# Kernel tuning notes

Hardware: AMD Instinct MI355X
Metric: run time of the kernel (lower is better)

Reference implementation:

```python
import jax, jax.numpy as jnp
import numpy as np

NUM_EMBEDDINGS = 1024
EMBEDDING_DIM = 256
COMMITMENT_COST = 0.25


def setup_inputs() -> dict:
    key = jax.random.key(0)
    k1, k2 = jax.random.split(key)
    inputs = jax.random.normal(k1, (32, EMBEDDING_DIM, 32, 32), dtype=jnp.float32)
    # codebook init matches torch: uniform(-1/K, 1/K)
    weight = jax.random.uniform(
        k2, (NUM_EMBEDDINGS, EMBEDDING_DIM), dtype=jnp.float32,
        minval=-1.0 / NUM_EMBEDDINGS, maxval=1.0 / NUM_EMBEDDINGS)
    return {"inputs": inputs, "weight": weight}


def reference(inputs, weight):
    # inputs: [B, C, H, W] with C == EMBEDDING_DIM; weight: [K, D]
    x = jnp.transpose(inputs, (0, 2, 3, 1))            # [B, H, W, D]
    input_shape = x.shape
    flat = x.reshape(-1, EMBEDDING_DIM)                # [N, D]

    distances = (jnp.sum(flat * flat, axis=1, keepdims=True)
                 + jnp.sum(weight * weight, axis=1)
                 - 2.0 * (flat @ weight.T))
    encoding_indices = jnp.argmin(distances, axis=1)   # [N]
    encodings = jax.nn.one_hot(encoding_indices, NUM_EMBEDDINGS, dtype=jnp.float32)  # [N, K]

    # one_hot @ weight == gather; use gather for efficiency (same values)
    quantized = weight[encoding_indices].reshape(input_shape)  # [B, H, W, D]

    e_latent_loss = jnp.mean((jax.lax.stop_gradient(quantized) - x) ** 2)
    q_latent_loss = jnp.mean((quantized - jax.lax.stop_gradient(x)) ** 2)
    loss = q_latent_loss + COMMITMENT_COST * e_latent_loss

    # straight-through estimator
    quantized_st = x + jax.lax.stop_gradient(quantized - x)

    avg_probs = jnp.mean(encodings, axis=0)            # [K]
    perplexity = jnp.exp(-jnp.sum(avg_probs * jnp.log(avg_probs + 1e-10)))

    return (loss,
            jnp.transpose(quantized_st, (0, 3, 1, 2)),  # back to [B, C, H, W]
            perplexity,
            encodings)
```

## Files before the change

kernel.cpp:

```cpp
#include <hip/hip_runtime.h>
#include <hip/hip_bf16.h>

#define HWDIM 1024
#define DDIM 256
#define KCODES 1024
#define NROWS 32768
#define BSTRIDE (DDIM * HWDIM)
#define GUARD 1.5e-4f

typedef __attribute__((ext_vector_type(8))) short short8;
typedef __attribute__((ext_vector_type(4))) float f32x4;
typedef unsigned long long ull;


__device__ __forceinline__ unsigned short f2bf(float v) {
  __hip_bfloat16 b = __float2bfloat16(v);
  return *reinterpret_cast<unsigned short*>(&b);
}
__device__ __forceinline__ float bf2f(unsigned short u) {
  __hip_bfloat16 b;
  *reinterpret_cast<unsigned short*>(&b) = u;
  return __bfloat162float(b);
}
__device__ __forceinline__ ull pk(float d, int k) {
  unsigned ub = __float_as_uint(d);
  ub = (ub & 0x80000000u) ? ~ub : (ub | 0x80000000u);
  return ((ull)ub << 32) | (unsigned)k;
}
__device__ __forceinline__ float keyq(ull key) {
  unsigned ub = (unsigned)(key >> 32);
  unsigned orig = (ub & 0x80000000u) ? (ub & 0x7FFFFFFFu) : ~ub;
  return __uint_as_float(orig);
}

__device__ __forceinline__ float pair128_sq(const float* p, int stride) {
  float a[8];
#pragma unroll
  for (int j = 0; j < 8; ++j) { float v = p[j * stride]; a[j] = __fmul_rn(v, v); }
  for (int i = 8; i < 128; i += 8) {
#pragma unroll
    for (int j = 0; j < 8; ++j) {
      float v = p[(i + j) * stride];
      a[j] = __fadd_rn(a[j], __fmul_rn(v, v));
    }
  }
  float s01 = __fadd_rn(a[0], a[1]), s23 = __fadd_rn(a[2], a[3]);
  float s45 = __fadd_rn(a[4], a[5]), s67 = __fadd_rn(a[6], a[7]);
  return __fadd_rn(__fadd_rn(s01, s23), __fadd_rn(s45, s67));
}

__global__ __launch_bounds__(256) void k_prep(
    const float* __restrict__ w, float* __restrict__ wT, float* __restrict__ ss,
    int* __restrict__ hist, double* __restrict__ loss,
    int* __restrict__ wcount, int* __restrict__ pcount,
    unsigned short* __restrict__ wh8, unsigned short* __restrict__ wl8) {
  __shared__ float tile[64][65];
  const int t = threadIdx.x;
  int g = blockIdx.x * 256 + t;
  {
    int k = g >> 5, oct = g & 31;
    const float* p = w + k * DDIM + oct * 8;
    short8 hv, lv;
#pragma unroll
    for (int j = 0; j < 8; ++j) {
      float v = p[j];
      unsigned short h = f2bf(v);
      unsigned short l = f2bf(__fsub_rn(v, bf2f(h)));
      hv[j] = (short)h; lv[j] = (short)l;
    }
    *(short8*)&wh8[oct * 8192 + k * 8] = hv;
    *(short8*)&wl8[oct * 8192 + k * 8] = lv;
  }
  if (g < KCODES) {
    hist[g] = 0;
    const float* p = w + g * DDIM;
    ss[g] = __fadd_rn(pair128_sq(p, 1), pair128_sq(p + 128, 1));
  }
  if (g == 0) { *loss = 0.0; *wcount = 0; *pcount = 0; }
  if (blockIdx.x < 64) {
    const int k0 = (blockIdx.x & 15) * 64, d0 = (blockIdx.x >> 4) * 64;
    const int c = t & 63, r = t >> 6;
#pragma unroll
    for (int m = 0; m < 16; ++m)
      tile[r + m * 4][c] = w[(k0 + r + m * 4) * DDIM + d0 + c];
    __syncthreads();
#pragma unroll
    for (int m = 0; m < 16; ++m)
      wT[(size_t)(d0 + r + m * 4) * KCODES + k0 + c] = tile[c][r + m * 4];
  }
}

__global__ __launch_bounds__(256) void k_argmfma(
    const float* __restrict__ in,
    const unsigned short* __restrict__ wh8, const unsigned short* __restrict__ wl8,
    const float* __restrict__ ss, unsigned* __restrict__ kkarr,
    int* __restrict__ wlist, int* __restrict__ wcount,
    int* __restrict__ plist, int* __restrict__ pcount) {
  __shared__ __align__(16) unsigned short Ah[32 * 64 * 8];
  __shared__ __align__(16) unsigned short Al[32 * 64 * 8];
  __shared__ ull best1[64], best2[64], best3[64];

  const int t = threadIdx.x;
  const int n0 = blockIdx.x * 64;
  const int b = n0 >> 10, hw0 = n0 & 1023;

  {
    const int hw = t & 63, dg = t >> 6;
    const float* xp = in + b * BSTRIDE + hw0 + hw;
#pragma unroll
    for (int dd = 0; dd < 64; dd += 2) {
      int d = dg * 64 + dd;
      float f0 = xp[d * HWDIM], f1 = xp[(d + 1) * HWDIM];
      unsigned short h0 = f2bf(f0);
      unsigned short l0 = f2bf(__fsub_rn(f0, bf2f(h0)));
      unsigned short h1 = f2bf(f1);
      unsigned short l1 = f2bf(__fsub_rn(f1, bf2f(h1)));
      int base = ((d >> 3) * 64 + hw) * 8 + (d & 7);
      *(unsigned*)&Ah[base] = (unsigned)h0 | ((unsigned)h1 << 16);
      *(unsigned*)&Al[base] = (unsigned)l0 | ((unsigned)l1 << 16);
    }
  }
  if (t < 64) { best1[t] = ~0ull; best2[t] = ~0ull; best3[t] = ~0ull; }
  __syncthreads();

  const int wv = t >> 6, ln = t & 63;
  const int rw = (wv & 1) * 32;
  const int cw = (wv >> 1) * 64;
  const int l15 = ln & 15, quad = ln >> 4;

  ull rb1[8], rb2[8], rb3[8];
#pragma unroll
  for (int i = 0; i < 8; ++i) { rb1[i] = ~0ull; rb2[i] = ~0ull; rb3[i] = ~0ull; }

  for (int kb = 0; kb < 8; ++kb) {
    const int cb = kb * 128 + cw;
    f32x4 acc[2][4];
#pragma unroll
    for (int rt = 0; rt < 2; ++rt)
#pragma unroll
      for (int ct = 0; ct < 4; ++ct) acc[rt][ct] = (f32x4){0.f, 0.f, 0.f, 0.f};

#pragma unroll
    for (int ki = 0; ki < 8; ++ki) {
      const int obase = ki * 4 + quad;
      short8 ah[2], al[2], bh[4], bl[4];
#pragma unroll
      for (int rt = 0; rt < 2; ++rt) {
        int row = rw + rt * 16 + l15;
        ah[rt] = *(const short8*)&Ah[(obase * 64 + row) * 8];
        al[rt] = *(const short8*)&Al[(obase * 64 + row) * 8];
      }
#pragma unroll
      for (int ct = 0; ct < 4; ++ct) {
        int off = obase * 8192 + (cb + ct * 16 + l15) * 8;
        bh[ct] = *(const short8*)&wh8[off];
        bl[ct] = *(const short8*)&wl8[off];
      }
#pragma unroll
      for (int rt = 0; rt < 2; ++rt)
#pragma unroll
        for (int ct = 0; ct < 4; ++ct) {
          acc[rt][ct] = __builtin_amdgcn_mfma_f32_16x16x32_bf16(ah[rt], bh[ct], acc[rt][ct], 0, 0, 0);
          acc[rt][ct] = __builtin_amdgcn_mfma_f32_16x16x32_bf16(ah[rt], bl[ct], acc[rt][ct], 0, 0, 0);
          acc[rt][ct] = __builtin_amdgcn_mfma_f32_16x16x32_bf16(al[rt], bh[ct], acc[rt][ct], 0, 0, 0);
        }
    }

    float sv[4];
#pragma unroll
    for (int ct = 0; ct < 4; ++ct) sv[ct] = ss[cb + ct * 16 + l15];
#pragma unroll
    for (int rt = 0; rt < 2; ++rt)
#pragma unroll
      for (int reg = 0; reg < 4; ++reg) {
        int idx = rt * 4 + reg;
        ull b1 = rb1[idx], b2 = rb2[idx], b3 = rb3[idx];
#pragma unroll
        for (int ct = 0; ct < 4; ++ct) {
          float q = fmaf(-2.f, acc[rt][ct][reg], sv[ct]);
          ull key = pk(q, cb + ct * 16 + l15);
          if (key < b1)      { b3 = b2; b2 = b1; b1 = key; }
          else if (key < b2) { b3 = b2; b2 = key; }
          else if (key < b3) { b3 = key; }
        }
        rb1[idx] = b1; rb2[idx] = b2; rb3[idx] = b3;
      }
  }

#pragma unroll
  for (int rt = 0; rt < 2; ++rt)
#pragma unroll
    for (int reg = 0; reg < 4; ++reg)
      atomicMin(&best1[rw + rt * 16 + quad * 4 + reg], rb1[rt * 4 + reg]);
  __syncthreads();
#pragma unroll
  for (int rt = 0; rt < 2; ++rt)
#pragma unroll
    for (int reg = 0; reg < 4; ++reg) {
      int row = rw + rt * 16 + quad * 4 + reg;
      int idx = rt * 4 + reg;
      ull sub = (rb1[idx] == best1[row]) ? rb2[idx] : rb1[idx];
      atomicMin(&best2[row], sub);
    }
  __syncthreads();
#pragma unroll
  for (int rt = 0; rt < 2; ++rt)
#pragma unroll
    for (int reg = 0; reg < 4; ++reg) {
      int row = rw + rt * 16 + quad * 4 + reg;
      int idx = rt * 4 + reg;
      ull b1 = best1[row], b2 = best2[row];
      ull c = (rb1[idx] != b1 && rb1[idx] != b2) ? rb1[idx]
            : ((rb2[idx] != b1 && rb2[idx] != b2) ? rb2[idx] : rb3[idx]);
      atomicMin(&best3[row], c);
    }
  __syncthreads();
  if (t < 64) {
    ull k1 = best1[t];
    kkarr[n0 + t] = (unsigned)(k1 & 0xFFFFFFFFull);
    float q1 = keyq(k1);
    if (!(keyq(best2[t]) - q1 > GUARD)) {
      if (keyq(best3[t]) - q1 > GUARD) {
        int p = atomicAdd(pcount, 1);
        plist[p] = (n0 + t) | ((int)(best2[t] & 0xFFFFFFFFull) << 16);
      } else {
        int p = atomicAdd(wcount, 1);
        wlist[p] = n0 + t;
      }
    }
  }
}

__global__ __launch_bounds__(256) void k_fallback(
    const float* __restrict__ in, const float* __restrict__ w,
    const float* __restrict__ wT, const float* __restrict__ ss,
    const int* __restrict__ wlist, const int* __restrict__ wcount,
    const int* __restrict__ plist, const int* __restrict__ pcount,
    unsigned* __restrict__ kkarr) {
  __shared__ float xrow[256];
  __shared__ float rsh;
  __shared__ ull bmin;
  __shared__ ull pkeys[2];
  const int t = threadIdx.x;

  const int pc = *pcount;
  for (int i = blockIdx.x; i < pc; i += gridDim.x) {
    const int pe = plist[i];
    const int n = pe & 0xFFFF;
    const unsigned k2 = ((unsigned)pe) >> 16;
    const unsigned k1 = kkarr[n];
    const int b = n >> 10, hw = n & 1023;
    xrow[t] = in[b * BSTRIDE + t * HWDIM + hw];
    __syncthreads();
    if (t == 0) rsh = __fadd_rn(pair128_sq(xrow, 1), pair128_sq(xrow + 128, 1));
    __syncthreads();
    if (t < 2) {
      unsigned k = t ? k2 : k1;
      const float* wr = w + (size_t)k * DDIM;
      float m = 0.f;
      for (int d = 0; d < 256; ++d) m = fmaf(xrow[d], wr[d], m);
      float dist = fmaf(-2.f, m, __fadd_rn(rsh, ss[k]));
      pkeys[t] = pk(dist, (int)k);
    }
    __syncthreads();
    if (t == 0) {
      ull kmin = pkeys[0] < pkeys[1] ? pkeys[0] : pkeys[1];
      kkarr[n] = (unsigned)(kmin & 0xFFFFFFFFull);
    }
    __syncthreads();
  }

  const int cnt = *wcount;
  for (int i = blockIdx.x; i < cnt; i += gridDim.x) {
    const int n = wlist[i];
    const int b = n >> 10, hw = n & 1023;
    xrow[t] = in[b * BSTRIDE + t * HWDIM + hw];
    if (t == 0) bmin = ~0ull;
    __syncthreads();
    if (t == 0) rsh = __fadd_rn(pair128_sq(xrow, 1), pair128_sq(xrow + 128, 1));
    __syncthreads();
    float m[4] = {0.f, 0.f, 0.f, 0.f};
    for (int d = 0; d < 256; ++d) {
      float xv = xrow[d];
      const float* wd = wT + (size_t)d * KCODES + t;
      m[0] = fmaf(xv, wd[0], m[0]);
      m[1] = fmaf(xv, wd[256], m[1]);
      m[2] = fmaf(xv, wd[512], m[2]);
      m[3] = fmaf(xv, wd[768], m[3]);
    }
    ull lb = ~0ull;
#pragma unroll
    for (int j = 0; j < 4; ++j) {
      int k = t + j * 256;
      float dist = fmaf(-2.f, m[j], __fadd_rn(rsh, ss[k]));
      ull key = pk(dist, k);
      if (key < lb) lb = key;
    }
    atomicMin(&bmin, lb);
    __syncthreads();
    if (t == 0) kkarr[n] = (unsigned)(bmin & 0xFFFFFFFFull);
    __syncthreads();
  }
}

__global__ __launch_bounds__(256) void k_quantenc(
    const float* __restrict__ in, const float* __restrict__ w,
    const unsigned* __restrict__ kkarr, int* __restrict__ hist,
    float* __restrict__ enc, float* __restrict__ outq, double* __restrict__ loss) {
  __shared__ float wrow[64][65];
  __shared__ unsigned kk[64];
  __shared__ double red[256];

  const int t = threadIdx.x;
  const int q = blockIdx.x & 3;
  const int n0 = (blockIdx.x >> 2) * 64;
  const int dc = q * 64;
  const int c0 = q * 256;
  const int b = n0 >> 10, hw0 = n0 & 1023;

  if (t < 64) kk[t] = kkarr[n0 + t];
  __syncthreads();

  if (q == 0 && t < 64) atomicAdd(&hist[kk[t]], 1);

#pragma unroll 4
  for (int m = 0; m < 32; ++m) {
    int u = m * 256 + t;
    int r = u >> 7, c2 = u & 127;
    int cbase = c0 + c2 * 2;
    unsigned kr = kk[r];
    float2 v;
    v.x = (cbase == (int)kr) ? 1.0f : 0.0f;
    v.y = (cbase + 1 == (int)kr) ? 1.0f : 0.0f;
    *(float2*)&enc[(size_t)(n0 + r) * 1024 + cbase] = v;
  }

#pragma unroll
  for (int m = 0; m < 16; ++m) {
    int u = t + m * 256;
    int r = u >> 6, dd = u & 63;
    wrow[r][dd] = w[kk[r] * DDIM + dc + dd];
  }
  __syncthreads();

  const float* inb = in + b * BSTRIDE + hw0;
  float* outb = outq + b * BSTRIDE + hw0;
  const int hwl = t & 63, dl = t >> 6;
  double lsum = 0.0;
#pragma unroll
  for (int dd = 0; dd < 64; dd += 4) {
    int d = dc + dd + dl;
    float x = inb[d * HWDIM + hwl];
    float wv = wrow[hwl][dd + dl];
    float diff = __fsub_rn(wv, x);
    outb[d * HWDIM + hwl] = __fadd_rn(x, diff);
    lsum += (double)diff * (double)diff;
  }
  red[t] = lsum;
  __syncthreads();
  for (int s = 128; s > 0; s >>= 1) {
    if (t < s) red[t] += red[t + s];
    __syncthreads();
  }
  if (t == 0) atomicAdd(loss, red[0]);
}

__global__ void k_final(const int* __restrict__ hist, const double* __restrict__ loss,
                        float* __restrict__ out) {
  __shared__ double red[256];
  int t = threadIdx.x;
  double s = 0.0;
  for (int i = t; i < KCODES; i += 256) {
    double p = (double)hist[i] * (1.0 / 32768.0);
    s += p * log(p + 1e-10);
  }
  red[t] = s;
  __syncthreads();
  for (int st = 128; st > 0; st >>= 1) {
    if (t < st) red[t] += red[t + st];
    __syncthreads();
  }
  if (t == 0) {
    out[8388609] = (float)exp(-red[0]);
    double m = *loss / 8388608.0;
    out[0] = (float)(1.25 * m);
  }
}

extern "C" void kernel_launch(void* const* d_in, const int* in_sizes, int n_in,
                              void* d_out, int out_size, void* d_ws, size_t ws_size,
                              hipStream_t stream) {
  const float* in = (const float*)d_in[0];
  const float* w  = (const float*)d_in[1];
  float* out = (float*)d_out;

  char* wsb = (char*)d_ws;
  float*    wT     = (float*)   (wsb + 0);
  float*    ssp    = (float*)   (wsb + 1048576);
  unsigned* kkarr  = (unsigned*)(wsb + 1052672);
  int*      wlist  = (int*)     (wsb + 1183744);
  int*      hist   = (int*)     (wsb + 1314816);
  int*      plist  = (int*)     (wsb + 1318912);
  double*   loss   = (double*)  (wsb + 1449984);
  int*      wcount = (int*)     (wsb + 1449992);
  int*      pcount = (int*)     (wsb + 1449996);

  char* ob = (char*)d_out + 33554448;
  unsigned short* wh8 = (unsigned short*)(ob + 0);
  unsigned short* wl8 = (unsigned short*)(ob + 524288);
  float* encp = out + 8388610;

  k_prep<<<dim3(128), dim3(256), 0, stream>>>(w, wT, ssp, hist, loss, wcount, pcount, wh8, wl8);
  k_argmfma<<<dim3(512), dim3(256), 0, stream>>>(in, wh8, wl8, ssp, kkarr,
                                                 wlist, wcount, plist, pcount);
  k_fallback<<<dim3(1024), dim3(256), 0, stream>>>(in, w, wT, ssp, wlist, wcount,
                                                   plist, pcount, kkarr);
  k_quantenc<<<dim3(2048), dim3(256), 0, stream>>>(in, w, kkarr, hist, encp,
                                                   out + 1, loss);
  k_final<<<dim3(1), dim3(256), 0, stream>>>(hist, loss, out);
}
```

Baseline: 342.1 us.

## Software-pipeline codebook fragment loads with register ring buffer in argmin MFMA kernel

After: 449.0 us. 1.31x slower.

```diff
diff --git a/kernel.cpp b/kernel.cpp
--- a/kernel.cpp
+++ b/kernel.cpp
@@ -90,7 +90,7 @@
   }
 }
 
-__global__ __launch_bounds__(256) void k_argmfma(
+__global__ __launch_bounds__(256, 2) void k_argmfma(
     const float* __restrict__ in,
     const unsigned short* __restrict__ wh8, const unsigned short* __restrict__ wl8,
     const float* __restrict__ ss, unsigned* __restrict__ kkarr,
@@ -98,19 +98,26 @@
     int* __restrict__ plist, int* __restrict__ pcount) {
   __shared__ __align__(16) unsigned short Ah[32 * 64 * 8];
   __shared__ __align__(16) unsigned short Al[32 * 64 * 8];
+  __shared__ __align__(16) float ss_l[1024];
   __shared__ ull best1[64], best2[64], best3[64];
 
   const int t = threadIdx.x;
   const int n0 = blockIdx.x * 64;
   const int b = n0 >> 10, hw0 = n0 & 1023;
 
+  const int wv = t >> 6, ln = t & 63;
+  const int rw = (wv & 1) * 32;
+  const int cw = (wv >> 1) * 64;
+  const int l15 = ln & 15, quad = ln >> 4;
+
   {
     const int hw = t & 63, dg = t >> 6;
     const float* xp = in + b * BSTRIDE + hw0 + hw;
 #pragma unroll
     for (int dd = 0; dd < 64; dd += 2) {
       int d = dg * 64 + dd;
-      float f0 = xp[d * HWDIM], f1 = xp[(d + 1) * HWDIM];
+      float f0 = __builtin_nontemporal_load(&xp[d * HWDIM]);
+      float f1 = __builtin_nontemporal_load(&xp[(d + 1) * HWDIM]);
       unsigned short h0 = f2bf(f0);
       unsigned short l0 = f2bf(__fsub_rn(f0, bf2f(h0)));
       unsigned short h1 = f2bf(f1);
@@ -120,13 +127,21 @@
       *(unsigned*)&Al[base] = (unsigned)l0 | ((unsigned)l1 << 16);
     }
   }
+  *(float4*)&ss_l[t * 4] = *(const float4*)&ss[t * 4];
   if (t < 64) { best1[t] = ~0ull; best2[t] = ~0ull; best3[t] = ~0ull; }
-  __syncthreads();
-
-  const int wv = t >> 6, ln = t & 63;
-  const int rw = (wv & 1) * 32;
-  const int cw = (wv >> 1) * 64;
-  const int l15 = ln & 15, quad = ln >> 4;
+
+  short8 bhB[4][4], blB[4][4];
+#pragma unroll
+  for (int p = 0; p < 4; ++p) {
+    const int obase = p * 4 + quad;
+#pragma unroll
+    for (int ct = 0; ct < 4; ++ct) {
+      int off = obase * 8192 + (cw + ct * 16 + l15) * 8;
+      bhB[p][ct] = *(const short8*)&wh8[off];
+      blB[p][ct] = *(const short8*)&wl8[off];
+    }
+  }
+  __syncthreads();
 
   ull rb1[8], rb2[8], rb3[8];
 #pragma unroll
@@ -142,33 +157,48 @@
 
 #pragma unroll
     for (int ki = 0; ki < 8; ++ki) {
+      const int slot = ki & 3;
       const int obase = ki * 4 + quad;
-      short8 ah[2], al[2], bh[4], bl[4];
+      short8 ah[2], al[2];
 #pragma unroll
       for (int rt = 0; rt < 2; ++rt) {
         int row = rw + rt * 16 + l15;
         ah[rt] = *(const short8*)&Ah[(obase * 64 + row) * 8];
         al[rt] = *(const short8*)&Al[(obase * 64 + row) * 8];
       }
-#pragma unroll
-      for (int ct = 0; ct < 4; ++ct) {
-        int off = obase * 8192 + (cb + ct * 16 + l15) * 8;
-        bh[ct] = *(const short8*)&wh8[off];
-        bl[ct] = *(const short8*)&wl8[off];
+      __builtin_amdgcn_s_setprio(1);
+#pragma unroll
+      for (int rt = 0; rt < 2; ++rt)
+#pragma unroll
+        for (int ct = 0; ct < 4; ++ct) {
+          acc[rt][ct] = __builtin_amdgcn_mfma_f32_16x16x32_bf16(ah[rt], bhB[slot][ct], acc[rt][ct], 0, 0, 0);
+          acc[rt][ct] = __builtin_amdgcn_mfma_f32_16x16x32_bf16(ah[rt], blB[slot][ct], acc[rt][ct], 0, 0, 0);
+          acc[rt][ct] = __builtin_amdgcn_mfma_f32_16x16x32_bf16(al[rt], bhB[slot][ct], acc[rt][ct], 0, 0, 0);
+        }
+      __builtin_amdgcn_s_setprio(0);
+      if (ki < 4) {
+        const int obase2 = (ki + 4) * 4 + quad;
+#pragma unroll
+        for (int ct = 0; ct < 4; ++ct) {
+          int off = obase2 * 8192 + (cb + ct * 16 + l15) * 8;
+          bhB[slot][ct] = *(const short8*)&wh8[off];
+          blB[slot][ct] = *(const short8*)&wl8[off];
+        }
+      } else if (kb < 7) {
+        const int obase2 = (ki - 4) * 4 + quad;
+        const int cb2 = cb + 128;
+#pragma unroll
+        for (int ct = 0; ct < 4; ++ct) {
+          int off = obase2 * 8192 + (cb2 + ct * 16 + l15) * 8;
+          bhB[slot][ct] = *(const short8*)&wh8[off];
+          blB[slot][ct] = *(const short8*)&wl8[off];
+        }
       }
-#pragma unroll
-      for (int rt = 0; rt < 2; ++rt)
-#pragma unroll
-        for (int ct = 0; ct < 4; ++ct) {
-          acc[rt][ct] = __builtin_amdgcn_mfma_f32_16x16x32_bf16(ah[rt], bh[ct], acc[rt][ct], 0, 0, 0);
-          acc[rt][ct] = __builtin_amdgcn_mfma_f32_16x16x32_bf16(ah[rt], bl[ct], acc[rt][ct], 0, 0, 0);
-          acc[rt][ct] = __builtin_amdgcn_mfma_f32_16x16x32_bf16(al[rt], bh[ct], acc[rt][ct], 0, 0, 0);
-        }
     }
 
     float sv[4];
 #pragma unroll
-    for (int ct = 0; ct < 4; ++ct) sv[ct] = ss[cb + ct * 16 + l15];
+    for (int ct = 0; ct < 4; ++ct) sv[ct] = ss_l[cb + ct * 16 + l15];
 #pragma unroll
     for (int rt = 0; rt < 2; ++rt)
 #pragma unroll
```
